# Kernel tuning notes

Measured on AMD Instinct MI355X. Metric: run time of the kernel, lower is better.

Reference implementation:

```python
import jax, jax.numpy as jnp
from jax import lax
import numpy as np

N_TOTAL = 262144
NUM_SAMPLE = 1024
KNN_K = 16
NUM_CLASSES = 13
HIDDEN = 128
EPS = 1e-8


def _sqdist(a, b):
    # (Na,3),(Nb,3) -> (Na,Nb) squared euclidean; same argmin as torch.cdist
    return (jnp.sum(a * a, axis=1)[:, None]
            + jnp.sum(b * b, axis=1)[None, :]
            - 2.0 * a @ b.T)


def _farthest_point_sample(xyz, n_samples):
    # sequential FPS starting from index 0 (deterministic start)
    n = xyz.shape[0]

    def step(carry, _):
        min_d2, last = carry
        d2 = jnp.sum((xyz - xyz[last]) ** 2, axis=-1)
        min_d2 = jnp.minimum(min_d2, d2)
        nxt = jnp.argmax(min_d2).astype(jnp.int32)
        return (min_d2, nxt), nxt

    init = (jnp.full((n,), 1e10, dtype=xyz.dtype), jnp.int32(0))
    _, idxs = lax.scan(step, init, None, length=n_samples - 1)
    return jnp.concatenate([jnp.zeros((1,), jnp.int32), idxs])


def _compute_normals(pts, k):
    # PCA normal per point from its k nearest neighbors (self excluded)
    d2 = _sqdist(pts, pts)                      # (S,S), S=1024 -> small
    _, nbr_idx = lax.top_k(-d2, k + 1)
    nbr = pts[nbr_idx[:, 1:]]                   # (S,k,3)
    centered = nbr - jnp.mean(nbr, axis=1, keepdims=True)
    cov = jnp.einsum('ski,skj->sij', centered, centered) / (k - 1)
    _, eigvecs = jnp.linalg.eigh(cov)           # ascending eigenvalues
    normal = eigvecs[..., 0]                    # smallest-eigval eigenvector
    return normal / (jnp.linalg.norm(normal, axis=-1, keepdims=True) + EPS)


def _forward(gaussian_positions, gaussian_colors, W1, b1, W2, b2, W3, b3):
    sample_idx = _farthest_point_sample(gaussian_positions, NUM_SAMPLE)
    dxyz = gaussian_positions[sample_idx]       # (S,3)
    drgb = gaussian_colors[sample_idx]          # (S,3)
    dnrm = _compute_normals(dxyz, KNN_K)        # (S,3)
    feats = jnp.concatenate([dxyz, drgb, dnrm], axis=1)  # (S,9)

    # pointwise segmentation network (stand-in for PointNet++ get_model)
    h = jax.nn.relu(feats @ W1 + b1)
    h = jax.nn.relu(h @ W2 + b2)
    pred = h @ W3 + b3                          # (S, num_classes)

    feat_down = jax.nn.softmax(pred, axis=1)
    lbl_down = jnp.argmax(pred, axis=1)

    # 1-NN label propagation: streaming-min candidate (memory-bound)
    d2_full = _sqdist(gaussian_positions, dxyz)  # (N, S) ~ 1 GB
    nearest = jnp.argmin(d2_full, axis=1)
    return feat_down[nearest], lbl_down[nearest]


def setup_inputs() -> dict:
    key = jax.random.key(0)
    ks = jax.random.split(key, 8)
    pos = jax.random.normal(ks[0], (N_TOTAL, 3), jnp.float32)
    col = jax.random.uniform(ks[1], (N_TOTAL, 3), jnp.float32)
    W1 = jax.random.normal(ks[2], (9, HIDDEN), jnp.float32) / np.sqrt(9.0)
    b1 = jnp.zeros((HIDDEN,), jnp.float32)
    W2 = jax.random.normal(ks[3], (HIDDEN, HIDDEN), jnp.float32) / np.sqrt(HIDDEN)
    b2 = jnp.zeros((HIDDEN,), jnp.float32)
    W3 = jax.random.normal(ks[4], (HIDDEN, NUM_CLASSES), jnp.float32) / np.sqrt(HIDDEN)
    b3 = jnp.zeros((NUM_CLASSES,), jnp.float32)
    return {"gaussian_positions": pos, "gaussian_colors": col,
            "W1": W1, "b1": b1, "W2": W2, "b2": b2, "W3": W3, "b3": b3}


def reference(gaussian_positions, gaussian_colors, W1, b1, W2, b2, W3, b3):
    return _forward(gaussian_positions, gaussian_colors, W1, b1, W2, b2, W3, b3)
```

## Files before the change

### kernel.cpp

```cpp
#include <hip/hip_runtime.h>
#include <math.h>

#define N_TOTAL    262144
#define NUM_SAMPLE 1024
#define FPS_BLOCKS 64
#define FPS_THREADS 256
#define FPS_PPT (N_TOTAL / (FPS_BLOCKS * FPS_THREADS))
#define M_WAVE 4
#define POOL (FPS_BLOCKS * 4 * M_WAVE)
#define ENT_PER_T (POOL / FPS_THREADS)
#define QD (POOL / 64)
#define SEL_CAP 1023

__device__ __forceinline__ float addrn(float a, float b) { return __fadd_rn(a, b); }
__device__ __forceinline__ float subrn(float a, float b) { return __fsub_rn(a, b); }
__device__ __forceinline__ float mulrn(float a, float b) { return __fmul_rn(a, b); }

__device__ __forceinline__ float d2rn(float ax, float ay, float az,
                                      float bx, float by, float bz) {
  float dx = subrn(ax, bx), dy = subrn(ay, by), dz = subrn(az, bz);
  return addrn(addrn(mulrn(dx, dx), mulrn(dy, dy)), mulrn(dz, dz));
}

__device__ __forceinline__ bool lex_gt(float m1, unsigned i1, float m2, unsigned i2) {
  return (m1 > m2) || (m1 == m2 && i1 > i2);
}
__device__ __forceinline__ bool lex_ge(float m1, unsigned i1, float m2, unsigned i2) {
  return (m1 > m2) || (m1 == m2 && i1 >= i2);
}

template <int CTRL>
__device__ __forceinline__ int dpp_i(int x) {
  return __builtin_amdgcn_update_dpp(x, x, CTRL, 0xF, 0xF, false);
}
__device__ __forceinline__ float wave_fmax_bcast(float v) {
  v = fmaxf(v, __int_as_float(dpp_i<0x111>(__float_as_int(v))));
  v = fmaxf(v, __int_as_float(dpp_i<0x112>(__float_as_int(v))));
  v = fmaxf(v, __int_as_float(dpp_i<0x114>(__float_as_int(v))));
  v = fmaxf(v, __int_as_float(dpp_i<0x118>(__float_as_int(v))));
  v = fmaxf(v, __int_as_float(dpp_i<0x142>(__float_as_int(v))));
  v = fmaxf(v, __int_as_float(dpp_i<0x143>(__float_as_int(v))));
  return __int_as_float(__builtin_amdgcn_readlane(__float_as_int(v), 63));
}
__device__ __forceinline__ unsigned wave_umax_bcast(unsigned v) {
  unsigned o;
  o = (unsigned)dpp_i<0x111>((int)v); v = (o > v) ? o : v;
  o = (unsigned)dpp_i<0x112>((int)v); v = (o > v) ? o : v;
  o = (unsigned)dpp_i<0x114>((int)v); v = (o > v) ? o : v;
  o = (unsigned)dpp_i<0x118>((int)v); v = (o > v) ? o : v;
  o = (unsigned)dpp_i<0x142>((int)v); v = (o > v) ? o : v;
  o = (unsigned)dpp_i<0x143>((int)v); v = (o > v) ? o : v;
  return (unsigned)__builtin_amdgcn_readlane((int)v, 63);
}

__device__ __forceinline__ float slapy2f(float x, float y) {
  float xa = fabsf(x), ya = fabsf(y);
  float w = fmaxf(xa, ya), z = fminf(xa, ya);
  if (z == 0.f) return w;
  float t = z / w;
  return w * __fsqrt_rn(1.f + t * t);
}

__device__ __forceinline__ void slartgf(float f, float g, float& c, float& s, float& r) {
  if (g == 0.f) { c = 1.f; s = 0.f; r = f; }
  else if (f == 0.f) { c = 0.f; s = (g > 0.f) ? 1.f : -1.f; r = fabsf(g); }
  else {
    float d = __fsqrt_rn(f * f + g * g);
    c = fabsf(f) / d;
    r = (f >= 0.f) ? d : -d;
    s = g / r;
  }
}

__device__ void slaev2f(float a, float b, float c0, float& rt1, float& rt2,
                        float& cs1, float& sn1) {
  float sm = a + c0, df = a - c0;
  float adf = fabsf(df), tb = b + b, ab = fabsf(tb);
  float acmx, acmn;
  if (fabsf(a) > fabsf(c0)) { acmx = a; acmn = c0; } else { acmx = c0; acmn = a; }
  float rt;
  if (adf > ab)      { float t = ab / adf; rt = adf * __fsqrt_rn(1.f + t * t); }
  else if (adf < ab) { float t = adf / ab; rt = ab * __fsqrt_rn(1.f + t * t); }
  else               { rt = ab * __fsqrt_rn(2.f); }
  int sgn1;
  if (sm < 0.f)      { rt1 = 0.5f * (sm - rt); sgn1 = -1; rt2 = (acmx / rt1) * acmn - (b / rt1) * b; }
  else if (sm > 0.f) { rt1 = 0.5f * (sm + rt); sgn1 = 1;  rt2 = (acmx / rt1) * acmn - (b / rt1) * b; }
  else               { rt1 = 0.5f * rt; rt2 = -0.5f * rt; sgn1 = 1; }
  float cs; int sgn2;
  if (df >= 0.f) { cs = df + rt; sgn2 = 1; } else { cs = df - rt; sgn2 = -1; }
  float acs = fabsf(cs);
  if (acs > ab) {
    float ct = -tb / cs;
    sn1 = 1.f / __fsqrt_rn(1.f + ct * ct);
    cs1 = ct * sn1;
  } else {
    if (ab == 0.f) { cs1 = 1.f; sn1 = 0.f; }
    else { float tn = -cs / tb; cs1 = 1.f / __fsqrt_rn(1.f + tn * tn); sn1 = tn * cs1; }
  }
  if (sgn1 == sgn2) { float tn = cs1; cs1 = -sn1; sn1 = tn; }
}

#define D_(i) d[(i)-1]
#define E_(i) e[(i)-1]

__device__ void ssteqr3(float d[3], float e[2], float Z[3][3]) {
  const float eps    = 5.9604645e-08f;
  const float eps2   = 3.5527137e-15f;
  const float safmin = 1.17549435e-38f;
  const float ssfmax = 3.0744573e+18f;
  const float ssfmin = 3.0517578e-05f;
  const int n = 3;
  int jtot = 0, nmaxit = 90;
  int l1 = 1;

  while (true) {
    if (l1 > n) break;
    if (l1 > 1) E_(l1 - 1) = 0.f;
    int m = n;
    for (int mm = l1; mm <= n - 1; ++mm) {
      float tst = fabsf(E_(mm));
      if (tst == 0.f) { m = mm; break; }
      if (tst <= (__fsqrt_rn(fabsf(D_(mm))) * __fsqrt_rn(fabsf(D_(mm + 1)))) * eps) {
        E_(mm) = 0.f; m = mm; break;
      }
    }
    int l = l1, lsv = l, lend = m, lendsv = m;
    l1 = m + 1;
    if (lend == l) continue;

    float anorm = fabsf(D_(lend));
    for (int i2 = l; i2 <= lend - 1; ++i2) {
      anorm = fmaxf(anorm, fabsf(D_(i2)));
      anorm = fmaxf(anorm, fabsf(E_(i2)));
    }
    int iscale = 0;
    if (anorm == 0.f) continue;
    if (anorm > ssfmax) {
      iscale = 1; float mul = ssfmax / anorm;
      for (int i2 = l; i2 <= lend; ++i2) D_(i2) *= mul;
      for (int i2 = l; i2 <= lend - 1; ++i2) E_(i2) *= mul;
    } else if (anorm < ssfmin) {
      iscale = 2; float mul = ssfmin / anorm;
      for (int i2 = l; i2 <= lend; ++i2) D_(i2) *= mul;
      for (int i2 = l; i2 <= lend - 1; ++i2) E_(i2) *= mul;
    }

    if (fabsf(D_(lend)) < fabsf(D_(l))) { int t = l; l = lend; lend = t; }

    if (lend > l) {
      while (true) {
        int m2 = lend;
        if (l != lend) {
          for (int mm = l; mm <= lend - 1; ++mm) {
            float tst = fabsf(E_(mm)); tst = tst * tst;
            if (tst <= (eps2 * fabsf(D_(mm))) * fabsf(D_(mm + 1)) + safmin) { m2 = mm; break; }
          }
        }
        if (m2 < lend) E_(m2) = 0.f;
        float p = D_(l);
        if (m2 == l) { D_(l) = p; l = l + 1; if (l <= lend) continue; break; }
        if (m2 == l + 1) {
          float rt1, rt2, cc, ss;
          slaev2f(D_(l), E_(l), D_(l + 1), rt1, rt2, cc, ss);
          for (int i2 = 0; i2 < 3; ++i2) {
            float tmp = Z[i2][l];
            Z[i2][l]     = cc * tmp - ss * Z[i2][l - 1];
            Z[i2][l - 1] = ss * tmp + cc * Z[i2][l - 1];
          }
          D_(l) = rt1; D_(l + 1) = rt2; E_(l) = 0.f;
          l = l + 2; if (l <= lend) continue; break;
        }
        if (jtot == nmaxit) break;
        ++jtot;
        float g = (D_(l + 1) - p) / (2.f * E_(l));
        float r = slapy2f(g, 1.f);
        float sgn_rg = (g >= 0.f) ? r : -r;
        g = D_(m2) - p + E_(l) / (g + sgn_rg);
        float s = 1.f, c = 1.f;
        p = 0.f;
        float csv[2], ssv[2];
        for (int i2 = m2 - 1; i2 >= l; --i2) {
          float f = s * E_(i2);
          float b = c * E_(i2);
          slartgf(g, f, c, s, r);
          if (i2 != m2 - 1) E_(i2 + 1) = r;
          g = D_(i2 + 1) - p;
          r = (D_(i2) - g) * s + 2.f * c * b;
          p = s * r;
          D_(i2 + 1) = g + p;
          g = c * r - b;
          csv[i2 - l] = c; ssv[i2 - l] = -s;
        }
        for (int j = m2 - 1; j >= l; --j) {
          float ct = csv[j - l], st = ssv[j - l];
          for (int i2 = 0; i2 < 3; ++i2) {
            float tmp = Z[i2][j];
            Z[i2][j]     = ct * tmp - st * Z[i2][j - 1];
            Z[i2][j - 1] = st * tmp + ct * Z[i2][j - 1];
          }
        }
        D_(l) = D_(l) - p;
        E_(l) = g;
      }
    } else {
      while (true) {
        int m2 = lend;
        if (l != lend) {
          for (int mm = l; mm >= lend + 1; --mm) {
            float tst = fabsf(E_(mm - 1)); tst = tst * tst;
            if (tst <= (eps2 * fabsf(D_(mm))) * fabsf(D_(mm - 1)) + safmin) { m2 = mm; break; }
          }
        }
        if (m2 > lend) E_(m2 - 1) = 0.f;
        float p = D_(l);
        if (m2 == l) { D_(l) = p; l = l - 1; if (l >= lend) continue; break; }
        if (m2 == l - 1) {
          float rt1, rt2, cc, ss;
          slaev2f(D_(l - 1), E_(l - 1), D_(l), rt1, rt2, cc, ss);
          for (int i2 = 0; i2 < 3; ++i2) {
            float tmp = Z[i2][l - 1];
            Z[i2][l - 1] = cc * tmp - ss * Z[i2][l - 2];
            Z[i2][l - 2] = ss * tmp + cc * Z[i2][l - 2];
          }
          D_(l - 1) = rt1; D_(l) = rt2; E_(l - 1) = 0.f;
          l = l - 2; if (l >= lend) continue; break;
        }
        if (jtot == nmaxit) break;
        ++jtot;
        float g = (D_(l - 1) - p) / (2.f * E_(l - 1));
        float r = slapy2f(g, 1.f);
        float sgn_rg = (g >= 0.f) ? r : -r;
        g = D_(m2) - p + E_(l - 1) / (g + sgn_rg);
        float s = 1.f, c = 1.f;
        p = 0.f;
        float csv[2], ssv[2];
        for (int i2 = m2; i2 <= l - 1; ++i2) {
          float f = s * E_(i2);
          float b = c * E_(i2);
          slartgf(g, f, c, s, r);
          if (i2 != m2) E_(i2 - 1) = r;
          g = D_(i2) - p;
          r = (D_(i2 + 1) - g) * s + 2.f * c * b;
          p = s * r;
          D_(i2) = g + p;
          g = c * r - b;
          csv[i2 - m2] = c; ssv[i2 - m2] = s;
        }
        for (int j = m2; j <= l - 1; ++j) {
          float ct = csv[j - m2], st = ssv[j - m2];
          for (int i2 = 0; i2 < 3; ++i2) {
            float tmp = Z[i2][j];
            Z[i2][j]     = ct * tmp - st * Z[i2][j - 1];
            Z[i2][j - 1] = st * tmp + ct * Z[i2][j - 1];
          }
        }
        D_(l) = D_(l) - p;
        E_(l - 1) = g;
      }
    }
    if (iscale == 1) {
      float mul = anorm / ssfmax;
      for (int i2 = lsv; i2 <= lendsv; ++i2) D_(i2) *= mul;
      for (int i2 = lsv; i2 <= lendsv - 1; ++i2) E_(i2) *= mul;
    } else if (iscale == 2) {
      float mul = anorm / ssfmin;
      for (int i2 = lsv; i2 <= lendsv; ++i2) D_(i2) *= mul;
      for (int i2 = lsv; i2 <= lendsv - 1; ++i2) E_(i2) *= mul;
    }
  }
  for (int ii = 2; ii <= n; ++ii) {
    int i2 = ii - 1, k = i2;
    float p = D_(i2);
    for (int j = ii; j <= n; ++j) if (D_(j) < p) { k = j; p = D_(j); }
    if (k != i2) {
      D_(k) = D_(i2); D_(i2) = p;
      for (int rr = 0; rr < 3; ++rr) {
        float t = Z[rr][i2 - 1]; Z[rr][i2 - 1] = Z[rr][k - 1]; Z[rr][k - 1] = t;
      }
    }
  }
}

__device__ void eigh3_smallest(float a00, float a10, float a20, float a11, float a21, float a22,
                               float& nx, float& ny, float& nz) {
  float d[3], e[2];
  float Z[3][3] = {{1.f,0.f,0.f},{0.f,1.f,0.f},{0.f,0.f,1.f}};
  float tau, v2;
  {
    float alpha = a10, x = a20;
    float xnorm = fabsf(x);
    if (xnorm == 0.f) {
      tau = 0.f; v2 = 0.f;
      d[0] = a00; d[1] = a11; d[2] = a22;
      e[0] = alpha; e[1] = a21;
    } else {
      float beta = -copysignf(slapy2f(alpha, x), alpha);
      tau = (beta - alpha) / beta;
      v2 = x / (alpha - beta);
      float w0 = (tau * a11) + tau * (a21 * v2);
      float w1 = (tau * a21) + (tau * v2) * a22;
      float ac = (-0.5f * tau) * (w0 + w1 * v2);
      w0 = w0 + ac;
      w1 = w1 + ac * v2;
      d[0] = a00;
      d[1] = (a11 - w0) - w0;
      d[2] = (a22 - v2 * w1) - w1 * v2;
      e[0] = beta;
      e[1] = (a21 - v2 * w0) - w1;
    }
  }
  ssteqr3(d, e, Z);
  if (tau != 0.f) {
    for (int c = 0; c < 3; ++c) {
      float w = Z[1][c] + Z[2][c] * v2;
      float temp = (-tau) * w;
      Z[1][c] = Z[1][c] + temp;
      Z[2][c] = Z[2][c] + v2 * temp;
    }
  }
  nx = Z[0][0]; ny = Z[1][0]; nz = Z[2][0];
}

__global__ void k0_init(unsigned long long* cand, int* sample_idx) {
  int t = blockIdx.x * blockDim.x + threadIdx.x;
  if (t < 2 * POOL) cand[t] = 0ull;
  if (t == 0) sample_idx[0] = 0;
}

__global__ __launch_bounds__(FPS_THREADS, 1) void k1_fps(
    const float* __restrict__ pos,
    unsigned long long* __restrict__ cand,
    int* __restrict__ sample_idx) {
  __shared__ float4 sel4[SEL_CAP];
  __shared__ float act_x[POOL], act_y[POOL], act_z[POOL], act_md[POOL];
  __shared__ unsigned act_idf[POOL];
  __shared__ float thrT_md[FPS_THREADS];
  __shared__ unsigned thrT_idf[FPS_THREADS];
  __shared__ int sh_pc;

  const int tidx = threadIdx.x;
  const int lane = tidx & 63;
  const int gtid = blockIdx.x * FPS_THREADS + tidx;

  float px[FPS_PPT], py[FPS_PPT], pz[FPS_PPT], md[FPS_PPT];
#pragma unroll
  for (int k = 0; k < FPS_PPT; ++k) {
    int p = gtid + k * (FPS_BLOCKS * FPS_THREADS);
    px[k] = pos[3 * p]; py[k] = pos[3 * p + 1]; pz[k] = pos[3 * p + 2];
    md[k] = 1e10f;
  }
  const unsigned idf0 = 0x3FFFFFu - (unsigned)gtid;
  if (tidx == 0) sel4[0] = make_float4(pos[0], pos[1], pos[2], 0.f);
  __syncthreads();
  int sel_cnt = 1, total = 0, bt = 0;
  while (total < NUM_SAMPLE - 1) {
    ++bt;
    {
      float4 sc = sel4[0];
      for (int s = 0; s < sel_cnt; ++s) {
        float4 sn = (s + 1 < sel_cnt) ? sel4[s + 1] : sc;
#pragma unroll
        for (int k = 0; k < FPS_PPT; ++k)
          md[k] = fminf(md[k], d2rn(px[k], py[k], pz[k], sc.x, sc.y, sc.z));
        sc = sn;
      }
    }
    const unsigned tag = (unsigned)bt & 1023u;
    unsigned long long* setbase = cand + (size_t)(bt & 1) * POOL;
    {
      float wmd[FPS_PPT];
#pragma unroll
      for (int k = 0; k < FPS_PPT; ++k) wmd[k] = md[k];
      unsigned long long mypub = 0ull;
      for (int r = 0; r < M_WAVE; ++r) {
        float bm = wmd[0]; unsigned bidf = idf0;
#pragma unroll
        for (int k = 1; k < FPS_PPT; ++k) {
          unsigned idfk = idf0 - ((unsigned)k << 14);
          if (wmd[k] > bm || (wmd[k] == bm && idfk > bidf)) { bm = wmd[k]; bidf = idfk; }
        }
        float wmx = wave_fmax_bcast(bm);
        unsigned tb = (bm == wmx) ? bidf : 0u;
        unsigned widf = wave_umax_bcast(tb);
        if (lane == r)
          mypub = ((unsigned long long)__float_as_uint(wmx) << 32) |
                  ((unsigned long long)widf << 10);
#pragma unroll
        for (int k = 0; k < FPS_PPT; ++k) {
          unsigned idfk = idf0 - ((unsigned)k << 14);
          if (wmd[k] == wmx && idfk == widf) wmd[k] = -1.f;
        }
      }
      if (lane < M_WAVE)
        __hip_atomic_store(setbase + blockIdx.x * (4 * M_WAVE) + (tidx >> 6) * M_WAVE + lane,
                           mypub | tag, __ATOMIC_RELAXED, __HIP_MEMORY_SCOPE_AGENT);
    }
    const int base_w = tidx * ENT_PER_T;
    {
      float cmd[ENT_PER_T]; unsigned cidf[ENT_PER_T];
      float cx[ENT_PER_T], cy[ENT_PER_T], cz[ENT_PER_T];
      unsigned done = 0;
      while (done != 0xFu) {
#pragma unroll
        for (int j = 0; j < ENT_PER_T; ++j) {
          if (!((done >> j) & 1u)) {
            unsigned long long v = __hip_atomic_load(setbase + base_w + j,
                                                     __ATOMIC_RELAXED, __HIP_MEMORY_SCOPE_AGENT);
            if ((unsigned)(v & 1023ull) == tag) {
              done |= 1u << j;
              cmd[j] = __uint_as_float((unsigned)(v >> 32));
              cidf[j] = (unsigned)((v >> 10) & 0x3FFFFFull);
              int gidx = 0x3FFFFF - (int)cidf[j];
              cx[j] = pos[3 * gidx]; cy[j] = pos[3 * gidx + 1]; cz[j] = pos[3 * gidx + 2];
            }
          }
        }
        if (done != 0xFu) __builtin_amdgcn_s_sleep(1);
      }
#pragma unroll
      for (int j = 0; j < ENT_PER_T; ++j) {
        int e = j * FPS_THREADS + tidx;
        act_x[e] = cx[j]; act_y[e] = cy[j]; act_z[e] = cz[j];
        act_md[e] = cmd[j]; act_idf[e] = cidf[j];
      }
      thrT_md[tidx] = cmd[ENT_PER_T - 1]; thrT_idf[tidx] = cidf[ENT_PER_T - 1];
    }
    __syncthreads();
    const int room = (NUM_SAMPLE - 1) - total;
    if (tidx < 64) {
      float q_md[QD], q_x[QD], q_y[QD], q_z[QD];
      unsigned q_idf[QD];
#pragma unroll
      for (int r = 0; r < QD; ++r) {
        int e2 = lane + 64 * r;
        q_x[r] = act_x[e2]; q_y[r] = act_y[e2]; q_z[r] = act_z[e2];
        q_md[r] = act_md[e2]; q_idf[r] = act_idf[e2];
      }
      float rm = thrT_md[lane]; unsigned ri = thrT_idf[lane];
#pragma unroll
      for (int r = 1; r < 4; ++r) {
        float m = thrT_md[lane + 64 * r]; unsigned ii = thrT_idf[lane + 64 * r];
        if (lex_gt(m, ii, rm, ri)) { rm = m; ri = ii; }
      }
      float Tmd = wave_fmax_bcast(rm);
      unsigned tbT = (rm == Tmd) ? ri : 0u;
      unsigned Tidf = wave_umax_bcast(tbT);

      int picks = 0;
      float X = 1e30f, Y = 1e30f, Z = 1e30f;
      for (;;) {
        float bm = -1.f; unsigned bidf = 0u;
        float bx = 0.f, by = 0.f, bz = 0.f;
#pragma unroll
        for (int j = 0; j < QD; ++j) {
          float nd = fminf(q_md[j], d2rn(q_x[j], q_y[j], q_z[j], X, Y, Z));
          q_md[j] = nd;
          if (lex_gt(nd, q_idf[j], bm, bidf)) {
            bm = nd; bidf = q_idf[j]; bx = q_x[j]; by = q_y[j]; bz = q_z[j];
          }
        }
        float wmx = wave_fmax_bcast(bm);
        unsigned long long ball = __ballot(bm == wmx);
        unsigned widf; int owner;
        if (__builtin_popcountll(ball) == 1) {
          owner = __builtin_ctzll(ball);
          widf = (unsigned)__builtin_amdgcn_readlane((int)bidf, owner);
        } else {
          unsigned tb = (bm == wmx) ? bidf : 0u;
          widf = wave_umax_bcast(tb);
          owner = __builtin_ctzll(__ballot(bm == wmx && bidf == widf));
        }
        if (picks >= room) break;
        if (!lex_ge(wmx, widf, Tmd, Tidf)) break;
        X = __int_as_float(__builtin_amdgcn_readlane(__float_as_int(bx), owner));
        Y = __int_as_float(__builtin_amdgcn_readlane(__float_as_int(by), owner));
        Z = __int_as_float(__builtin_amdgcn_readlane(__float_as_int(bz), owner));
        if (lane == 0) {
          sel4[picks] = make_float4(X, Y, Z, 0.f);
          if (blockIdx.x == 0) sample_idx[1 + total + picks] = 0x3FFFFF - (int)widf;
        }
        ++picks;
      }
      if (lane == 0) sh_pc = picks;
    }
    __syncthreads();
    sel_cnt = sh_pc;
    total += sel_cnt;
  }
}

__global__ __launch_bounds__(256) void k2a_knn(
    const float* __restrict__ pos, const float* __restrict__ col,
    const int* __restrict__ sample_idx,
    float4* __restrict__ sp4g, float* __restrict__ feats9) {
  __shared__ float4 sp[NUM_SAMPLE];
  const int tid = threadIdx.x, lane = tid & 63, wv = tid >> 6;
  for (int i = tid; i < NUM_SAMPLE; i += 256) {
    int idx = sample_idx[i];
    float x = pos[3 * idx], y = pos[3 * idx + 1], z = pos[3 * idx + 2];
    float nrm = addrn(addrn(mulrn(x, x), mulrn(y, y)), mulrn(z, z));
    float4 v = make_float4(x, y, z, nrm);
    sp[i] = v;
    if (blockIdx.x == 0) sp4g[i] = v;
  }
  __syncthreads();
  for (int it = 0; it < 4; ++it) {
    const int r = blockIdx.x * 16 + wv * 4 + it;
    float4 pr = sp[r];
    unsigned long long kk[16];
#pragma unroll
    for (int k = 0; k < 16; ++k) {
      int j = lane + 64 * k;
      float4 q = sp[j];
      float dot = fmaf(pr.z, q.z, fmaf(pr.y, q.y, mulrn(pr.x, q.x)));
      float d2 = subrn(addrn(pr.w, q.w), mulrn(2.f, dot));
      unsigned b = __float_as_uint(d2);
      unsigned sbits = (b & 0x80000000u) ? ~b : (b | 0x80000000u);
      kk[k] = ((unsigned long long)sbits << 32) | (unsigned)j;
    }
    int bi[17];
#pragma unroll
    for (int rsel = 0; rsel < 17; ++rsel) {
      unsigned long long best = 0xFFFFFFFFFFFFFFFFull;
#pragma unroll
      for (int k = 0; k < 16; ++k) best = (kk[k] < best) ? kk[k] : best;
#pragma unroll
      for (int mk = 1; mk < 64; mk <<= 1) {
        unsigned long long o = (unsigned long long)__shfl_xor((long long)best, mk, 64);
        best = (o < best) ? o : best;
      }
      int j = (int)(best & 0xFFFFFFFFull);
      bi[rsel] = j;
#pragma unroll
      for (int k = 0; k < 16; ++k)
        if (((j >> 6) == k) && ((j & 63) == lane)) kk[k] = 0xFFFFFFFFFFFFFFFFull;
    }
    float mx = 0.f, my = 0.f, mz = 0.f;
#pragma unroll
    for (int k = 1; k <= 16; ++k) {
      float4 q = sp[bi[k]];
      mx = addrn(mx, q.x); my = addrn(my, q.y); mz = addrn(mz, q.z);
    }
    mx = mulrn(mx, 0.0625f); my = mulrn(my, 0.0625f); mz = mulrn(mz, 0.0625f);
    float c00 = 0.f, c01 = 0.f, c02 = 0.f, c11 = 0.f, c12 = 0.f, c22 = 0.f;
#pragma unroll
    for (int k = 1; k <= 16; ++k) {
      float4 q = sp[bi[k]];
      float dx = subrn(q.x, mx), dy = subrn(q.y, my), dz = subrn(q.z, mz);
      c00 = addrn(c00, mulrn(dx, dx)); c01 = addrn(c01, mulrn(dx, dy));
      c02 = addrn(c02, mulrn(dx, dz)); c11 = addrn(c11, mulrn(dy, dy));
      c12 = addrn(c12, mulrn(dy, dz)); c22 = addrn(c22, mulrn(dz, dz));
    }
    c00 /= 15.f; c01 /= 15.f; c02 /= 15.f; c11 /= 15.f; c12 /= 15.f; c22 /= 15.f;

    float n0, n1, n2;
    eigh3_smallest(c00, c01, c02, c11, c12, c22, n0, n1, n2);
    float nn = __fsqrt_rn(addrn(addrn(mulrn(n0, n0), mulrn(n1, n1)), mulrn(n2, n2)));
    float den = addrn(nn, 1e-8f);
    n0 /= den; n1 /= den; n2 /= den;

    if (lane == 0) {
      int myidx = sample_idx[r];
      float* f = feats9 + r * 9;
      f[0] = pr.x; f[1] = pr.y; f[2] = pr.z;
      f[3] = col[3 * myidx]; f[4] = col[3 * myidx + 1]; f[5] = col[3 * myidx + 2];
      f[6] = n0; f[7] = n1; f[8] = n2;
    }
  }
}

__global__ __launch_bounds__(64) void k2b_mlp(
    const float* __restrict__ W1, const float* __restrict__ b1,
    const float* __restrict__ W2, const float* __restrict__ b2,
    const float* __restrict__ W3, const float* __restrict__ b3,
    const float* __restrict__ feats9,
    float* __restrict__ featd, int* __restrict__ lbl) {
  __shared__ float hbuf[64][129];
  const int tid = threadIdx.x;
  const int r = blockIdx.x * 64 + tid;
  float f9[9];
#pragma unroll
  for (int k = 0; k < 9; ++k) f9[k] = feats9[r * 9 + k];
  for (int jo = 0; jo < 128; ++jo) {
    float acc = 0.f;
#pragma unroll
    for (int k = 0; k < 9; ++k) acc = fmaf(f9[k], W1[k * 128 + jo], acc);
    acc += b1[jo];
    hbuf[tid][jo] = fmaxf(acc, 0.f);
  }
  float pd[13];
#pragma unroll
  for (int c = 0; c < 13; ++c) pd[c] = 0.f;
  for (int io = 0; io < 128; io += 16) {
    float acc[16];
#pragma unroll
    for (int t = 0; t < 16; ++t) acc[t] = 0.f;
    for (int j = 0; j < 128; ++j) {
      float hj = hbuf[tid][j];
#pragma unroll
      for (int t = 0; t < 16; ++t) acc[t] = fmaf(hj, W2[j * 128 + io + t], acc[t]);
    }
#pragma unroll
    for (int t = 0; t < 16; ++t) {
      float h2 = fmaxf(acc[t] + b2[io + t], 0.f);
#pragma unroll
      for (int c = 0; c < 13; ++c) pd[c] = fmaf(h2, W3[(io + t) * 13 + c], pd[c]);
    }
  }
#pragma unroll
  for (int c = 0; c < 13; ++c) pd[c] += b3[c];
  float mmax = pd[0];
#pragma unroll
  for (int c = 1; c < 13; ++c) mmax = fmaxf(mmax, pd[c]);
  float es = 0.f, ev[13];
#pragma unroll
  for (int c = 0; c < 13; ++c) { ev[c] = expf(pd[c] - mmax); es += ev[c]; }
#pragma unroll
  for (int c = 0; c < 13; ++c) featd[r * 13 + c] = ev[c] / es;
  int am = 0; float bv = pd[0];
#pragma unroll
  for (int c = 1; c < 13; ++c) { if (pd[c] > bv) { bv = pd[c]; am = c; } }
  lbl[r] = am;
}

__global__ __launch_bounds__(256) void k3_assign(
    const float* __restrict__ pos,
    const float4* __restrict__ sp4g,
    const float* __restrict__ featd,
    const int* __restrict__ lbl,
    float* __restrict__ out) {
  __shared__ float4 sp[NUM_SAMPLE];
  for (int i = threadIdx.x; i < NUM_SAMPLE; i += 256) sp[i] = sp4g[i];
  __syncthreads();
  int i = blockIdx.x * 256 + threadIdx.x;
  float x = pos[3 * i], y = pos[3 * i + 1], z = pos[3 * i + 2];
  float an = addrn(addrn(mulrn(x, x), mulrn(y, y)), mulrn(z, z));
  float bestd = 3.402823466e+38f; int bestj = 0;
#pragma unroll 4
  for (int j = 0; j < NUM_SAMPLE; ++j) {
    float4 q = sp[j];
    float dot = fmaf(z, q.z, fmaf(y, q.y, mulrn(x, q.x)));
    float d2 = subrn(addrn(an, q.w), mulrn(2.f, dot));
    if (d2 < bestd) { bestd = d2; bestj = j; }
  }
  const float* fr = featd + bestj * 13;
  float* o = out + (size_t)i * 13;
#pragma unroll
  for (int c = 0; c < 13; ++c) o[c] = fr[c];
  out[(size_t)N_TOTAL * 13 + i] = (float)lbl[bestj];
}

extern "C" void kernel_launch(void* const* d_in, const int* in_sizes, int n_in,
                              void* d_out, int out_size, void* d_ws, size_t ws_size,
                              hipStream_t stream) {
  (void)in_sizes; (void)n_in; (void)out_size; (void)ws_size;
  const float* pos = (const float*)d_in[0];
  const float* col = (const float*)d_in[1];
  const float* W1 = (const float*)d_in[2];
  const float* b1 = (const float*)d_in[3];
  const float* W2 = (const float*)d_in[4];
  const float* b2 = (const float*)d_in[5];
  const float* W3 = (const float*)d_in[6];
  const float* b3 = (const float*)d_in[7];
  float* out = (float*)d_out;

  char* w = (char*)d_ws;
  unsigned long long* cand = (unsigned long long*)(w);
  int* sample_idx = (int*)(w + 65536);
  float4* sp4g = (float4*)(w + 73728);
  float* featd = (float*)(w + 90112);
  int* lbl = (int*)(w + 143360);
  float* feats9 = (float*)(w + 147456);

  k0_init<<<16, 256, 0, stream>>>(cand, sample_idx);
  k1_fps<<<FPS_BLOCKS, FPS_THREADS, 0, stream>>>(pos, cand, sample_idx);
  k2a_knn<<<64, 256, 0, stream>>>(pos, col, sample_idx, sp4g, feats9);
  k2b_mlp<<<16, 64, 0, stream>>>(W1, b1, W2, b2, W3, b3, feats9, featd, lbl);
  k3_assign<<<N_TOTAL / 256, 256, 0, stream>>>(pos, sp4g, featd, lbl, out);
}
```

Before: 1.710 ms.

## Double per-wave candidate pool and split local FPS selection across two waves

```diff
diff --git a/kernel.cpp b/kernel.cpp
--- a/kernel.cpp
+++ b/kernel.cpp
@@ -6,10 +6,10 @@
 #define FPS_BLOCKS 64
 #define FPS_THREADS 256
 #define FPS_PPT (N_TOTAL / (FPS_BLOCKS * FPS_THREADS))
-#define M_WAVE 4
+#define M_WAVE 8
 #define POOL (FPS_BLOCKS * 4 * M_WAVE)
 #define ENT_PER_T (POOL / FPS_THREADS)
-#define QD (POOL / 64)
+#define QD 16
 #define SEL_CAP 1023
 
 __device__ __forceinline__ float addrn(float a, float b) { return __fadd_rn(a, b); }
@@ -336,6 +336,9 @@
   __shared__ unsigned act_idf[POOL];
   __shared__ float thrT_md[FPS_THREADS];
   __shared__ unsigned thrT_idf[FPS_THREADS];
+  __shared__ float sh_xmd[2], sh_xx[2], sh_xy[2], sh_xz[2];
+  __shared__ unsigned sh_xidf[2];
+  __shared__ int sh_seq[2];
   __shared__ int sh_pc;
 
   const int tidx = threadIdx.x;
@@ -400,7 +403,7 @@
       float cmd[ENT_PER_T]; unsigned cidf[ENT_PER_T];
       float cx[ENT_PER_T], cy[ENT_PER_T], cz[ENT_PER_T];
       unsigned done = 0;
-      while (done != 0xFu) {
+      while (done != 0xFFu) {
 #pragma unroll
         for (int j = 0; j < ENT_PER_T; ++j) {
           if (!((done >> j) & 1u)) {
@@ -415,7 +418,7 @@
             }
           }
         }
-        if (done != 0xFu) __builtin_amdgcn_s_sleep(1);
+        if (done != 0xFFu) __builtin_amdgcn_s_sleep(1);
       }
 #pragma unroll
       for (int j = 0; j < ENT_PER_T; ++j) {
@@ -424,15 +427,18 @@
         act_md[e] = cmd[j]; act_idf[e] = cidf[j];
       }
       thrT_md[tidx] = cmd[ENT_PER_T - 1]; thrT_idf[tidx] = cidf[ENT_PER_T - 1];
+      if (tidx == 0) { sh_seq[0] = 0; sh_seq[1] = 0; }
     }
     __syncthreads();
     const int room = (NUM_SAMPLE - 1) - total;
-    if (tidx < 64) {
+    if (tidx < 128) {
+      const int w = tidx >> 6;
+      const int ow = 1 - w;
       float q_md[QD], q_x[QD], q_y[QD], q_z[QD];
       unsigned q_idf[QD];
 #pragma unroll
       for (int r = 0; r < QD; ++r) {
-        int e2 = lane + 64 * r;
+        int e2 = w * (64 * QD) + lane + 64 * r;
         q_x[r] = act_x[e2]; q_y[r] = act_y[e2]; q_z[r] = act_z[e2];
         q_md[r] = act_md[e2]; q_idf[r] = act_idf[e2];
       }
@@ -446,6 +452,7 @@
       unsigned tbT = (rm == Tmd) ? ri : 0u;
       unsigned Tidf = wave_umax_bcast(tbT);
 
+      volatile int* vseq = (volatile int*)sh_seq;
       int picks = 0;
       float X = 1e30f, Y = 1e30f, Z = 1e30f;
       for (;;) {
@@ -470,18 +477,31 @@
           widf = wave_umax_bcast(tb);
           owner = __builtin_ctzll(__ballot(bm == wmx && bidf == widf));
         }
+        float WX = __int_as_float(__builtin_amdgcn_readlane(__float_as_int(bx), owner));
+        float WY = __int_as_float(__builtin_amdgcn_readlane(__float_as_int(by), owner));
+        float WZ = __int_as_float(__builtin_amdgcn_readlane(__float_as_int(bz), owner));
+        if (lane == 0) {
+          sh_xmd[w] = wmx; sh_xidf[w] = widf;
+          sh_xx[w] = WX; sh_xy[w] = WY; sh_xz[w] = WZ;
+          __threadfence_block();
+          vseq[w] = picks + 1;
+        }
+        while (vseq[ow] < picks + 1) { }
+        __threadfence_block();
+        float omd = sh_xmd[ow]; unsigned oidf = sh_xidf[ow];
+        float ox = sh_xx[ow], oy = sh_xy[ow], oz = sh_xz[ow];
+        bool mine = lex_gt(wmx, widf, omd, oidf);
+        float Wm = mine ? wmx : omd; unsigned Wi = mine ? widf : oidf;
+        X = mine ? WX : ox; Y = mine ? WY : oy; Z = mine ? WZ : oz;
         if (picks >= room) break;
-        if (!lex_ge(wmx, widf, Tmd, Tidf)) break;
-        X = __int_as_float(__builtin_amdgcn_readlane(__float_as_int(bx), owner));
-        Y = __int_as_float(__builtin_amdgcn_readlane(__float_as_int(by), owner));
-        Z = __int_as_float(__builtin_amdgcn_readlane(__float_as_int(bz), owner));
-        if (lane == 0) {
+        if (!lex_ge(Wm, Wi, Tmd, Tidf)) break;
+        if (w == 0 && lane == 0) {
           sel4[picks] = make_float4(X, Y, Z, 0.f);
-          if (blockIdx.x == 0) sample_idx[1 + total + picks] = 0x3FFFFF - (int)widf;
+          if (blockIdx.x == 0) sample_idx[1 + total + picks] = 0x3FFFFF - (int)Wi;
         }
         ++picks;
       }
-      if (lane == 0) sh_pc = picks;
+      if (tidx == 0) sh_pc = picks;
     }
     __syncthreads();
     sel_cnt = sh_pc;
```

New measurement: 1.999 ms. +16.9%, slower.

## Double per-wave candidate pool with lazily updated LDS tier for FPS batch picks

Applied to the files above, without the earlier changes.

```diff
diff --git a/kernel.cpp b/kernel.cpp
--- a/kernel.cpp
+++ b/kernel.cpp
@@ -6,10 +6,11 @@
 #define FPS_BLOCKS 64
 #define FPS_THREADS 256
 #define FPS_PPT (N_TOTAL / (FPS_BLOCKS * FPS_THREADS))
-#define M_WAVE 4
+#define M_WAVE 8
 #define POOL (FPS_BLOCKS * 4 * M_WAVE)
 #define ENT_PER_T (POOL / FPS_THREADS)
-#define QD (POOL / 64)
+#define QD 16
+#define LTIER 1024
 #define SEL_CAP 1023
 
 __device__ __forceinline__ float addrn(float a, float b) { return __fadd_rn(a, b); }
@@ -400,7 +401,7 @@
       float cmd[ENT_PER_T]; unsigned cidf[ENT_PER_T];
       float cx[ENT_PER_T], cy[ENT_PER_T], cz[ENT_PER_T];
       unsigned done = 0;
-      while (done != 0xFu) {
+      while (done != 0xFFu) {
 #pragma unroll
         for (int j = 0; j < ENT_PER_T; ++j) {
           if (!((done >> j) & 1u)) {
@@ -415,7 +416,7 @@
             }
           }
         }
-        if (done != 0xFu) __builtin_amdgcn_s_sleep(1);
+        if (done != 0xFFu) __builtin_amdgcn_s_sleep(1);
       }
 #pragma unroll
       for (int j = 0; j < ENT_PER_T; ++j) {
@@ -446,6 +447,33 @@
       unsigned tbT = (rm == Tmd) ? ri : 0u;
       unsigned Tidf = wave_umax_bcast(tbT);
 
+      float c_lmd = -1.f, c_lx = 0.f, c_ly = 0.f, c_lz = 0.f;
+      unsigned c_lidf = 0u; int c_lslot = LTIER;
+      auto lscan = [&]() {
+        float bm2 = -1.f; unsigned bidf2 = 0u; int bs2 = LTIER + lane;
+#pragma unroll
+        for (int r = 0; r < 16; ++r) {
+          int sl = LTIER + lane + 64 * r;
+          float m = act_md[sl]; unsigned ii = act_idf[sl];
+          if (lex_gt(m, ii, bm2, bidf2)) { bm2 = m; bidf2 = ii; bs2 = sl; }
+        }
+        float wm2 = wave_fmax_bcast(bm2);
+        unsigned long long ball2 = __ballot(bm2 == wm2);
+        unsigned wi2; int own2;
+        if (__builtin_popcountll(ball2) == 1) {
+          own2 = __builtin_ctzll(ball2);
+          wi2 = (unsigned)__builtin_amdgcn_readlane((int)bidf2, own2);
+        } else {
+          unsigned tb2 = (bm2 == wm2) ? bidf2 : 0u;
+          wi2 = wave_umax_bcast(tb2);
+          own2 = __builtin_ctzll(__ballot(bm2 == wm2 && bidf2 == wi2));
+        }
+        int slot = __builtin_amdgcn_readlane(bs2, own2);
+        c_lmd = wm2; c_lidf = wi2; c_lslot = slot;
+        c_lx = act_x[slot]; c_ly = act_y[slot]; c_lz = act_z[slot];
+      };
+      int lastp = 0;
+      lscan();
       int picks = 0;
       float X = 1e30f, Y = 1e30f, Z = 1e30f;
       for (;;) {
@@ -470,16 +498,46 @@
           widf = wave_umax_bcast(tb);
           owner = __builtin_ctzll(__ballot(bm == wmx && bidf == widf));
         }
+        float WX = __int_as_float(__builtin_amdgcn_readlane(__float_as_int(bx), owner));
+        float WY = __int_as_float(__builtin_amdgcn_readlane(__float_as_int(by), owner));
+        float WZ = __int_as_float(__builtin_amdgcn_readlane(__float_as_int(bz), owner));
+        bool ldsWins = lex_gt(c_lmd, c_lidf, wmx, widf);
+        if (ldsWins && lastp < picks) {
+          for (int r0 = 0; r0 < 16; r0 += 4) {
+            float mm[4], xx[4], yy[4], zz[4];
+#pragma unroll
+            for (int u = 0; u < 4; ++u) {
+              int sl = LTIER + lane + 64 * (r0 + u);
+              mm[u] = act_md[sl]; xx[u] = act_x[sl]; yy[u] = act_y[sl]; zz[u] = act_z[sl];
+            }
+            for (int p = lastp; p < picks; ++p) {
+              float4 s = sel4[p];
+#pragma unroll
+              for (int u = 0; u < 4; ++u)
+                mm[u] = fminf(mm[u], d2rn(xx[u], yy[u], zz[u], s.x, s.y, s.z));
+            }
+#pragma unroll
+            for (int u = 0; u < 4; ++u)
+              act_md[LTIER + lane + 64 * (r0 + u)] = mm[u];
+          }
+          lastp = picks;
+          lscan();
+          ldsWins = lex_gt(c_lmd, c_lidf, wmx, widf);
+        }
+        float Wm = ldsWins ? c_lmd : wmx;
+        unsigned Wi = ldsWins ? c_lidf : widf;
         if (picks >= room) break;
-        if (!lex_ge(wmx, widf, Tmd, Tidf)) break;
-        X = __int_as_float(__builtin_amdgcn_readlane(__float_as_int(bx), owner));
-        Y = __int_as_float(__builtin_amdgcn_readlane(__float_as_int(by), owner));
-        Z = __int_as_float(__builtin_amdgcn_readlane(__float_as_int(bz), owner));
+        if (!lex_ge(Wm, Wi, Tmd, Tidf)) break;
+        X = ldsWins ? c_lx : WX;
+        Y = ldsWins ? c_ly : WY;
+        Z = ldsWins ? c_lz : WZ;
         if (lane == 0) {
           sel4[picks] = make_float4(X, Y, Z, 0.f);
-          if (blockIdx.x == 0) sample_idx[1 + total + picks] = 0x3FFFFF - (int)widf;
+          if (blockIdx.x == 0) sample_idx[1 + total + picks] = 0x3FFFFF - (int)Wi;
+          if (ldsWins) act_md[c_lslot] = -1.f;
         }
         ++picks;
+        if (ldsWins) lscan();
       }
       if (lane == 0) sh_pc = picks;
     }
```

Result: slower. 2.226 ms (+30.2%).

## Merge candidate lists across wave pairs before publishing to global pool

Applied to the files above, without the earlier changes.

```diff
diff --git a/kernel.cpp b/kernel.cpp
--- a/kernel.cpp
+++ b/kernel.cpp
@@ -6,8 +6,9 @@
 #define FPS_BLOCKS 64
 #define FPS_THREADS 256
 #define FPS_PPT (N_TOTAL / (FPS_BLOCKS * FPS_THREADS))
-#define M_WAVE 4
-#define POOL (FPS_BLOCKS * 4 * M_WAVE)
+#define M_WAVE 8
+#define NPAIR (FPS_BLOCKS * 2)
+#define POOL (NPAIR * M_WAVE)
 #define ENT_PER_T (POOL / FPS_THREADS)
 #define QD (POOL / 64)
 #define SEL_CAP 1023
@@ -336,6 +337,8 @@
   __shared__ unsigned act_idf[POOL];
   __shared__ float thrT_md[FPS_THREADS];
   __shared__ unsigned thrT_idf[FPS_THREADS];
+  __shared__ float pairm[2][8];
+  __shared__ unsigned pairi[2][8];
   __shared__ int sh_pc;
 
   const int tidx = threadIdx.x;
@@ -367,11 +370,12 @@
     }
     const unsigned tag = (unsigned)bt & 1023u;
     unsigned long long* setbase = cand + (size_t)(bt & 1) * POOL;
+    const int wv = tidx >> 6;
+    float savm = -1.f; unsigned savi = 0u;
     {
       float wmd[FPS_PPT];
 #pragma unroll
       for (int k = 0; k < FPS_PPT; ++k) wmd[k] = md[k];
-      unsigned long long mypub = 0ull;
       for (int r = 0; r < M_WAVE; ++r) {
         float bm = wmd[0]; unsigned bidf = idf0;
 #pragma unroll
@@ -381,21 +385,41 @@
         }
         float wmx = wave_fmax_bcast(bm);
         unsigned tb = (bm == wmx) ? bidf : 0u;
+        unsigned widf = wave_umax_bcast(tb);
+        if (lane == r) { savm = wmx; savi = widf; }
+#pragma unroll
+        for (int k = 0; k < FPS_PPT; ++k) {
+          unsigned idfk = idf0 - ((unsigned)k << 14);
+          if (wmd[k] == wmx && idfk == widf) wmd[k] = -1.f;
+        }
+      }
+      if ((wv & 1) && lane < M_WAVE) {
+        pairm[wv >> 1][lane] = savm;
+        pairi[wv >> 1][lane] = savi;
+      }
+    }
+    __syncthreads();
+    if (!(wv & 1)) {
+      float cm = (lane < 8) ? savm
+               : ((lane < 16) ? pairm[wv >> 1][lane - 8] : -1.f);
+      unsigned ci = (lane < 8) ? savi
+               : ((lane < 16) ? pairi[wv >> 1][lane - 8] : 0u);
+      unsigned long long mypub = 0ull;
+      for (int r = 0; r < M_WAVE; ++r) {
+        float wmx = wave_fmax_bcast(cm);
+        unsigned tb = (cm == wmx) ? ci : 0u;
         unsigned widf = wave_umax_bcast(tb);
         if (lane == r)
           mypub = ((unsigned long long)__float_as_uint(wmx) << 32) |
                   ((unsigned long long)widf << 10);
-#pragma unroll
-        for (int k = 0; k < FPS_PPT; ++k) {
-          unsigned idfk = idf0 - ((unsigned)k << 14);
-          if (wmd[k] == wmx && idfk == widf) wmd[k] = -1.f;
-        }
-      }
-      if (lane < M_WAVE)
-        __hip_atomic_store(setbase + blockIdx.x * (4 * M_WAVE) + (tidx >> 6) * M_WAVE + lane,
+        if (cm == wmx && ci == widf) cm = -1.f;
+      }
+      if (lane < M_WAVE) {
+        int pair = 2 * blockIdx.x + (wv >> 1);
+        __hip_atomic_store(setbase + pair * M_WAVE + lane,
                            mypub | tag, __ATOMIC_RELAXED, __HIP_MEMORY_SCOPE_AGENT);
-    }
-    const int base_w = tidx * ENT_PER_T;
+      }
+    }
     {
       float cmd[ENT_PER_T]; unsigned cidf[ENT_PER_T];
       float cx[ENT_PER_T], cy[ENT_PER_T], cz[ENT_PER_T];
@@ -404,7 +428,7 @@
 #pragma unroll
         for (int j = 0; j < ENT_PER_T; ++j) {
           if (!((done >> j) & 1u)) {
-            unsigned long long v = __hip_atomic_load(setbase + base_w + j,
+            unsigned long long v = __hip_atomic_load(setbase + j * FPS_THREADS + tidx,
                                                      __ATOMIC_RELAXED, __HIP_MEMORY_SCOPE_AGENT);
             if ((unsigned)(v & 1023ull) == tag) {
               done |= 1u << j;
@@ -423,7 +447,13 @@
         act_x[e] = cx[j]; act_y[e] = cy[j]; act_z[e] = cz[j];
         act_md[e] = cmd[j]; act_idf[e] = cidf[j];
       }
-      thrT_md[tidx] = cmd[ENT_PER_T - 1]; thrT_idf[tidx] = cidf[ENT_PER_T - 1];
+      float tm = -1.f; unsigned ti = 0u;
+      if ((tidx & 7) == 7) {
+#pragma unroll
+        for (int j = 0; j < ENT_PER_T; ++j)
+          if (lex_gt(cmd[j], cidf[j], tm, ti)) { tm = cmd[j]; ti = cidf[j]; }
+      }
+      thrT_md[tidx] = tm; thrT_idf[tidx] = ti;
     }
     __syncthreads();
     const int room = (NUM_SAMPLE - 1) - total;
@@ -672,7 +702,7 @@
   int* lbl = (int*)(w + 143360);
   float* feats9 = (float*)(w + 147456);
 
-  k0_init<<<16, 256, 0, stream>>>(cand, sample_idx);
+  k0_init<<<8, 256, 0, stream>>>(cand, sample_idx);
   k1_fps<<<FPS_BLOCKS, FPS_THREADS, 0, stream>>>(pos, cand, sample_idx);
   k2a_knn<<<64, 256, 0, stream>>>(pos, col, sample_idx, sp4g, feats9);
   k2b_mlp<<<16, 64, 0, stream>>>(W1, b1, W2, b2, W3, b3, feats9, featd, lbl);
```

Measured after the change: 1.769 ms. +3.5%, slower.
